# Kernel optimization log

Hardware: AMD Instinct MI355X
Metric: run time of the kernel (lower is better)

The kernel has to match this reference:

```python
import jax, jax.numpy as jnp
import numpy as np

CODEBOOK_SIZE = 8192
TOKEN_SIZE = 256
COMMITMENT_COST = 0.25
B, C, H, W = 32, 256, 32, 32


def setup_inputs() -> dict:
    key = jax.random.key(0)
    k1, k2 = jax.random.split(key)
    z = jax.random.normal(k1, (B, C, H, W), dtype=jnp.float32)
    # torch init: uniform_(-1/codebook_size, 1/codebook_size)
    embedding = jax.random.uniform(
        k2, (CODEBOOK_SIZE, TOKEN_SIZE), dtype=jnp.float32,
        minval=-1.0 / CODEBOOK_SIZE, maxval=1.0 / CODEBOOK_SIZE)
    return {"z": z, "embedding": embedding}


def reference(z, embedding):
    # b c h w -> b h w c
    z = jnp.transpose(z.astype(jnp.float32), (0, 2, 3, 1))
    b, h, w, c = z.shape
    z_flat = z.reshape(-1, c)  # [N, c]

    # squared euclidean distances: ||z||^2 + ||e||^2 - 2 z e^T
    d = (jnp.sum(z_flat ** 2, axis=1, keepdims=True)
         + jnp.sum(embedding ** 2, axis=1)
         - 2.0 * jnp.einsum('nd,kd->nk', z_flat, embedding))  # [N, K]
    idx = jnp.argmin(d, axis=1)  # [N]

    z_q = embedding[idx].reshape(z.shape)  # [b,h,w,c]

    commitment_loss = COMMITMENT_COST * jnp.mean(
        (jax.lax.stop_gradient(z_q) - z) ** 2)
    codebook_loss = jnp.mean((z_q - jax.lax.stop_gradient(z)) ** 2)
    loss = commitment_loss + codebook_loss

    # straight-through estimator
    z_q_st = z + jax.lax.stop_gradient(z_q - z)
    z_q_out = jnp.transpose(z_q_st, (0, 3, 1, 2))  # b h w c -> b c h w

    min_encoding_indices = idx.reshape(b, h, w)
    return (z_q_out, loss, commitment_loss, codebook_loss,
            min_encoding_indices)
```

## Files before the change

### kernel.cpp

```cpp
#include <hip/hip_runtime.h>
#include <float.h>

#define NBATCH 32
#define NCHAN  256
#define NHW    1024
#define NTOK   32768
#define NK     8192
#define ND     256
#define ZELEMS 8388608
#define OUT_LOSS 8388608
#define OUT_IDX  8388611
#define MARGIN   1.2e-4f

typedef short bf16x8  __attribute__((ext_vector_type(8)));
typedef float f32x4   __attribute__((ext_vector_type(4)));
typedef float f32x16  __attribute__((ext_vector_type(16)));

__device__ __forceinline__ void gl_lds16(const void* g, void* l) {
    __builtin_amdgcn_global_load_lds(
        (const __attribute__((address_space(1))) unsigned int*)g,
        (__attribute__((address_space(3))) unsigned int*)l, 16, 0, 0);
}

__device__ __forceinline__ unsigned short f2bf(float f) {
    unsigned int u = __float_as_uint(f);
    u += 0x7FFFu + ((u >> 16) & 1u);
    return (unsigned short)(u >> 16);
}

__device__ __forceinline__ float embed8(float x, int code) {
    return __int_as_float((__float_as_int(x) & 0xFFFFFF00) | code);
}


__global__ __launch_bounds__(256) void k_en(const float* __restrict__ E,
                                            float* __restrict__ en,
                                            float* __restrict__ acc,
                                            int* __restrict__ counter) {
    int t = threadIdx.x;
    int wv = t >> 6, lane = t & 63;
    int k = blockIdx.x * 4 + wv;
    const float4* E4 = (const float4*)E;
    float4 v = E4[k * 64 + lane];
    float s = v.x * v.x + v.y * v.y + v.z * v.z + v.w * v.w;
    #pragma unroll
    for (int off = 32; off > 0; off >>= 1) s += __shfl_down(s, off, 64);
    if (lane == 0) en[k] = s;
    if (blockIdx.x == 0 && t == 0) { acc[0] = 0.0f; counter[0] = 0; }
}

__global__ __launch_bounds__(256) void k_castE(const float* __restrict__ E,
                                               unsigned short* __restrict__ Epre) {
    int g = blockIdx.x * 256 + threadIdx.x;
    int code = g >> 5, c16 = g & 31;
    int kc = c16 >> 2, qlog = c16 & 3;
    int row = code & 127, tile = code >> 7;
    const float4* E4 = (const float4*)(E + code * ND + c16 * 8);
    float4 a = E4[0], b = E4[1];
    unsigned int u[4];
    u[0] = (unsigned int)f2bf(a.x) | ((unsigned int)f2bf(a.y) << 16);
    u[1] = (unsigned int)f2bf(a.z) | ((unsigned int)f2bf(a.w) << 16);
    u[2] = (unsigned int)f2bf(b.x) | ((unsigned int)f2bf(b.y) << 16);
    u[3] = (unsigned int)f2bf(b.z) | ((unsigned int)f2bf(b.w) << 16);
    int p = (qlog + (row >> 1)) & 3;
    *(uint4*)((char*)Epre + (size_t)(tile * 8 + kc) * 8192 + row * 64 + p * 16) =
        make_uint4(u[0], u[1], u[2], u[3]);
}

__global__ __launch_bounds__(256) void k_castZ(const float* __restrict__ zg,
                                               unsigned short* __restrict__ Zpre) {
    __shared__ unsigned short buf[128][34];
    int bi = blockIdx.x;
    int b = bi >> 6, kc = (bi >> 3) & 7, hwt = bi & 7;
    int c0 = kc * 32, hw0 = hwt * 128;
    int t = threadIdx.x;
    #pragma unroll
    for (int r = 0; r < 4; ++r) {
        int idx = r * 256 + t;
        int c = idx >> 5, q = idx & 31;
        float4 v = *(const float4*)&zg[(b * 256 + c0 + c) * 1024 + hw0 + q * 4];
        buf[q * 4 + 0][c] = f2bf(v.x);
        buf[q * 4 + 1][c] = f2bf(v.y);
        buf[q * 4 + 2][c] = f2bf(v.z);
        buf[q * 4 + 3][c] = f2bf(v.w);
    }
    __syncthreads();
    int row = t >> 1, half = t & 1;
    char* base = (char*)Zpre + (size_t)((b * 8 + hwt) * 8 + kc) * 8192 + row * 64;
    #pragma unroll
    for (int s = 0; s < 2; ++s) {
        int qlog = half * 2 + s;
        unsigned int u[4];
        #pragma unroll
        for (int k = 0; k < 4; ++k) {
            int cc = qlog * 8 + 2 * k;
            u[k] = (unsigned int)buf[row][cc] | ((unsigned int)buf[row][cc + 1] << 16);
        }
        int p = (qlog + (row >> 1)) & 3;
        *(uint4*)(base + p * 16) = make_uint4(u[0], u[1], u[2], u[3]);
    }
}

__global__ __launch_bounds__(256, 2) void k_dist(const unsigned short* __restrict__ Epre,
                                                 const unsigned short* __restrict__ Zpre,
                                                 const float* __restrict__ en,
                                                 float2* __restrict__ part2) {
    __shared__ __align__(16) char smem[2 * 24576];
    __shared__ float2 red[2][128];
    __shared__ float en_s[256];

    const int t    = threadIdx.x;
    const int kbb  = blockIdx.x;
    const int mb   = blockIdx.y;
    const int n0   = mb * 128;
    const int w    = t >> 6, lane = t & 63;
    const int l31  = lane & 31, lhi = lane >> 5;
    const int wm   = w >> 1, wn = w & 1;
    const int cA   = (lhi + (l31 >> 1)) & 3;

    en_s[t] = en[kbb * 256 + t];

    const char* Ebase = (const char*)Epre + (size_t)(kbb * 2) * 65536;
    const char* Zbase = (const char*)Zpre + (size_t)mb * 65536;

    auto stage = [&](int kc, int buf) {
        char* db = smem + buf * 24576;
        #pragma unroll
        for (int r = 0; r < 6; ++r) {
            int s = w * 6 + r;
            const char* src;
            if (s < 8)       src = Ebase + kc * 8192 + s * 1024;
            else if (s < 16) src = Ebase + 65536 + kc * 8192 + (s - 8) * 1024;
            else             src = Zbase + kc * 8192 + (s - 16) * 1024;
            gl_lds16(src + lane * 16, db + s * 1024 + lane * 16);
        }
    };

    f32x16 acc[2][2][2];
    #pragma unroll
    for (int kt = 0; kt < 2; ++kt)
        #pragma unroll
        for (int i = 0; i < 2; ++i)
            #pragma unroll
            for (int j = 0; j < 2; ++j) acc[kt][i][j] = (f32x16)0.0f;

    const int rowEoff = (wm * 64 + l31) * 64;
    const int rowZoff = 16384 + (wn * 64 + l31) * 64;
    const int colk[2] = { (cA & 3) * 16, (cA ^ 2) * 16 };

    stage(0, 0);
    for (int kc = 0; kc < 8; ++kc) {
        __syncthreads();
        if (kc < 7) stage(kc + 1, (kc + 1) & 1);
        char* db = smem + (kc & 1) * 24576;

        bf16x8 ea[2][2][2], zb[2][2];
        #pragma unroll
        for (int ks = 0; ks < 2; ++ks) {
            #pragma unroll
            for (int kt = 0; kt < 2; ++kt)
                #pragma unroll
                for (int i = 0; i < 2; ++i)
                    ea[kt][i][ks] = *(const bf16x8*)(db + kt * 8192 + rowEoff
                                                     + i * 2048 + colk[ks]);
            #pragma unroll
            for (int j = 0; j < 2; ++j)
                zb[j][ks] = *(const bf16x8*)(db + rowZoff + j * 2048 + colk[ks]);
        }
        #pragma unroll
        for (int kt = 0; kt < 2; ++kt)
            #pragma unroll
            for (int ks = 0; ks < 2; ++ks)
                #pragma unroll
                for (int i = 0; i < 2; ++i)
                    #pragma unroll
                    for (int j = 0; j < 2; ++j)
                        acc[kt][i][j] = __builtin_amdgcn_mfma_f32_32x32x16_bf16(
                            ea[kt][i][ks], zb[j][ks], acc[kt][i][j], 0, 0, 0);
    }

    float v1[2] = { FLT_MAX, FLT_MAX }, v2[2] = { FLT_MAX, FLT_MAX };
    #pragma unroll
    for (int kt = 0; kt < 2; ++kt)
        #pragma unroll
        for (int i = 0; i < 2; ++i) {
            const int cb = (kt << 7) | (wm << 6) | (i << 5) | (lhi << 2);
            #pragma unroll
            for (int rq = 0; rq < 4; ++rq) {
                f32x4 ev = *(const f32x4*)&en_s[cb + 8 * rq];
                #pragma unroll
                for (int rr = 0; rr < 4; ++rr) {
                    const int r = rq * 4 + rr;
                    const int code = cb + 8 * rq + rr;
                    #pragma unroll
                    for (int j = 0; j < 2; ++j) {
                        float s  = fmaf(-2.0f, acc[kt][i][j][r], ev[rr]);
                        float se = embed8(s, code);
                        v2[j] = __builtin_amdgcn_fmed3f(se, v1[j], v2[j]);
                        v1[j] = fminf(v1[j], se);
                    }
                }
            }
        }
    #pragma unroll
    for (int j = 0; j < 2; ++j) {
        float b1 = __shfl_xor(v1[j], 32, 64);
        float b2 = __shfl_xor(v2[j], 32, 64);
        float hi = fmaxf(v1[j], b1);
        v1[j] = fminf(v1[j], b1);
        v2[j] = fminf(fminf(hi, v2[j]), b2);
    }
    if (lane < 32) {
        #pragma unroll
        for (int j = 0; j < 2; ++j)
            red[wm][wn * 64 + j * 32 + lane] = make_float2(v1[j], v2[j]);
    }
    __syncthreads();
    if (t < 128) {
        float2 A = red[0][t], B = red[1][t];
        float g1 = fminf(A.x, B.x);
        float g2 = fminf(fminf(fmaxf(A.x, B.x), A.y), B.y);
        part2[(size_t)(n0 + t) * 32 + kbb] = make_float2(g1, g2);
    }
}

__global__ __launch_bounds__(256) void k_refine(const float* __restrict__ zg,
                                                const float* __restrict__ E,
                                                const float2* __restrict__ part2,
                                                int* __restrict__ idxw,
                                                float* __restrict__ outF) {
    const int w = threadIdx.x >> 6, l = threadIdx.x & 63;
    const int n = blockIdx.x * 4 + w;
    const int b = n >> 10, hw = n & 1023;
    const float* zrow = zg + b * (NCHAN * NHW) + hw;

    float zreg[4];
    #pragma unroll
    for (int j = 0; j < 4; ++j) zreg[j] = zrow[(4 * l + j) * NHW];

    double z2 = 0.0;
    #pragma unroll
    for (int j = 0; j < 4; ++j) z2 += (double)zreg[j] * (double)zreg[j];
    #pragma unroll
    for (int m = 1; m < 64; m <<= 1) z2 += __shfl_xor(z2, m, 64);
    const float z2f = (float)z2;

    float2 p = make_float2(FLT_MAX, FLT_MAX);
    if (l < 32) p = part2[(size_t)n * 32 + l];
    int code1 = (l << 8) | (__float_as_int(p.x) & 0xFF);
    int code2 = (l << 8) | (__float_as_int(p.y) & 0xFF);

    float vmin = p.x;
    #pragma unroll
    for (int m = 1; m < 64; m <<= 1) vmin = fminf(vmin, __shfl_xor(vmin, m, 64));
    const float thr = vmin + MARGIN;

    unsigned long long m1 = __ballot(l < 32 && p.x <= thr);
    unsigned long long m2 = __ballot(l < 32 && p.y <= thr);

    float bdq = FLT_MAX; int bidx = 0x7fffffff;
    #pragma unroll
    for (int pass = 0; pass < 2; ++pass) {
        unsigned long long mm = pass ? m2 : m1;
        int ibits = pass ? code2 : code1;
        while (mm) {
            int src = __ffsll(mm) - 1; mm &= mm - 1;
            int cidx = __shfl(ibits, src, 64);
            const float4 e4 = *(const float4*)&E[cidx * ND + 4 * l];
            double g = (double)zreg[0] * (double)e4.x + (double)zreg[1] * (double)e4.y
                     + (double)zreg[2] * (double)e4.z + (double)zreg[3] * (double)e4.w;
            #pragma unroll
            for (int mk = 1; mk < 64; mk <<= 1) g += __shfl_xor(g, mk, 64);
            float c  = (float)(2.0 * g);
            float dq = z2f - c;
            if (dq < bdq || (dq == bdq && cidx < bidx)) { bdq = dq; bidx = cidx; }
        }
    }
    if (l == 0) { idxw[n] = bidx; outF[OUT_IDX + n] = (float)bidx; }
}

__global__ __launch_bounds__(256) void k_gather(const float* __restrict__ E,
                                                const float* __restrict__ zg,
                                                const int* __restrict__ idxw,
                                                float* __restrict__ out,
                                                float* __restrict__ acc,
                                                int* __restrict__ counter) {
    __shared__ __align__(16) float Es[64 * 256];
    __shared__ int sidx[64];
    __shared__ float wred[4];
    const int t = threadIdx.x;
    const int b = blockIdx.x >> 4, ht = blockIdx.x & 15;

    if (t < 64) sidx[t] = idxw[b * 1024 + ht * 64 + t];
    __syncthreads();
    const float4* E4 = (const float4*)E;
    #pragma unroll
    for (int r = 0; r < 16; ++r) {
        int li = r * 256 + t;
        int row = li >> 6, slot = li & 63;
        float4 v = E4[(size_t)sidx[row] * 64 + slot];
        *(float4*)&Es[row * 256 + ((slot ^ (row & 15)) * 4)] = v;
    }
    __syncthreads();

    const int hw = t & 63, wv = t >> 6;
    float s = 0.0f;
    #pragma unroll 8
    for (int cc = 0; cc < 64; ++cc) {
        int c = wv * 64 + cc;
        float e = Es[hw * 256 + (((c >> 2) ^ (hw & 15)) * 4) + (c & 3)];
        size_t gi = (size_t)(b * 256 + c) * 1024 + ht * 64 + hw;
        float zv = zg[gi];
        out[gi] = e;
        float d = e - zv;
        s = fmaf(d, d, s);
    }
    #pragma unroll
    for (int off = 32; off > 0; off >>= 1) s += __shfl_down(s, off, 64);
    if ((t & 63) == 0) wred[wv] = s;
    __syncthreads();
    if (t == 0) {
        atomicAdd(acc, wred[0] + wred[1] + wred[2] + wred[3]);
        __threadfence();
        int old = atomicAdd(counter, 1);
        if (old == 511) {
            float total = atomicAdd(acc, 0.0f);
            float mse = total / 8388608.0f;
            out[OUT_LOSS + 0] = 1.25f * mse;
            out[OUT_LOSS + 1] = 0.25f * mse;
            out[OUT_LOSS + 2] = mse;
        }
    }
}

extern "C" void kernel_launch(void* const* d_in, const int* in_sizes, int n_in,
                              void* d_out, int out_size, void* d_ws, size_t ws_size,
                              hipStream_t stream) {
    const float* zg = (const float*)d_in[0];
    const float* E  = (const float*)d_in[1];
    float* out = (float*)d_out;
    float* wsf = (float*)d_ws;
    float*  acc     = wsf;
    int*    counter = (int*)(wsf + 1);
    float*  en      = wsf + 64;
    int*    idxw    = (int*)(wsf + 64 + NK);
    float2* part2   = (float2*)(wsf + 64 + NK + NTOK);
    unsigned short* Epre = (unsigned short*)(wsf + 64 + NK + NTOK + 2097152);
    unsigned short* Zpre = (unsigned short*)d_out;

    k_en    <<<NK / 4, 256, 0, stream>>>(E, en, acc, counter);
    k_castE <<<1024, 256, 0, stream>>>(E, Epre);
    k_castZ <<<2048, 256, 0, stream>>>(zg, Zpre);
    k_dist  <<<dim3(32, 256), 256, 0, stream>>>(Epre, Zpre, en, part2);
    k_refine<<<NTOK / 4, 256, 0, stream>>>(zg, E, part2, idxw, out);
    k_gather<<<512, 256, 0, stream>>>(E, zg, idxw, out, acc, counter);
}
```

Measured before the change: 348.0 us.

## Restructure VQ distance pipeline: register-resident codebook, smaller tiles, fused norms, batched refine

Folds the codebook-norm computation into the bf16 cast kernel, which removes one launch. Both packed layouts change to an MFMA-fragment-friendly order. The distance kernel now loads codebook fragments straight from global memory into registers with double buffering and stages only Z through LDS. It uses 128-code tiles, a doubled grid and 3 blocks per CU, which changes how much data each block reuses. The refine kernel transposes a 64-token z tile through shared memory so reads are coalesced instead of strided per token. The trade-off is more partial-minimum entries per token, twice as many codebook tiles read, and less reuse of Z per block.

After: 318.9 us. 1.09x faster.

```diff
diff --git a/kernel.cpp b/kernel.cpp
--- a/kernel.cpp
+++ b/kernel.cpp
@@ -33,38 +33,30 @@
 }
 
 
-__global__ __launch_bounds__(256) void k_en(const float* __restrict__ E,
-                                            float* __restrict__ en,
-                                            float* __restrict__ acc,
-                                            int* __restrict__ counter) {
-    int t = threadIdx.x;
-    int wv = t >> 6, lane = t & 63;
-    int k = blockIdx.x * 4 + wv;
-    const float4* E4 = (const float4*)E;
-    float4 v = E4[k * 64 + lane];
-    float s = v.x * v.x + v.y * v.y + v.z * v.z + v.w * v.w;
-    #pragma unroll
-    for (int off = 32; off > 0; off >>= 1) s += __shfl_down(s, off, 64);
-    if (lane == 0) en[k] = s;
-    if (blockIdx.x == 0 && t == 0) { acc[0] = 0.0f; counter[0] = 0; }
-}
-
 __global__ __launch_bounds__(256) void k_castE(const float* __restrict__ E,
-                                               unsigned short* __restrict__ Epre) {
+                                               unsigned short* __restrict__ Epre,
+                                               float* __restrict__ en,
+                                               float* __restrict__ acc,
+                                               int* __restrict__ counter) {
     int g = blockIdx.x * 256 + threadIdx.x;
     int code = g >> 5, c16 = g & 31;
-    int kc = c16 >> 2, qlog = c16 & 3;
-    int row = code & 127, tile = code >> 7;
+    int kc = c16 >> 2, ks = (c16 >> 1) & 1, lhi = c16 & 1;
     const float4* E4 = (const float4*)(E + code * ND + c16 * 8);
     float4 a = E4[0], b = E4[1];
+    float s = a.x*a.x + a.y*a.y + a.z*a.z + a.w*a.w
+            + b.x*b.x + b.y*b.y + b.z*b.z + b.w*b.w;
+    #pragma unroll
+    for (int off = 1; off < 32; off <<= 1) s += __shfl_xor(s, off, 64);
+    if ((threadIdx.x & 31) == 0) en[code] = s;
     unsigned int u[4];
     u[0] = (unsigned int)f2bf(a.x) | ((unsigned int)f2bf(a.y) << 16);
     u[1] = (unsigned int)f2bf(a.z) | ((unsigned int)f2bf(a.w) << 16);
     u[2] = (unsigned int)f2bf(b.x) | ((unsigned int)f2bf(b.y) << 16);
     u[3] = (unsigned int)f2bf(b.z) | ((unsigned int)f2bf(b.w) << 16);
-    int p = (qlog + (row >> 1)) & 3;
-    *(uint4*)((char*)Epre + (size_t)(tile * 8 + kc) * 8192 + row * 64 + p * 16) =
+    *(uint4*)((char*)Epre + (size_t)(code >> 7) * 65536 + kc * 8192
+              + (ks * 2 + lhi) * 2048 + (code & 127) * 16) =
         make_uint4(u[0], u[1], u[2], u[3]);
+    if (blockIdx.x == 0 && threadIdx.x == 0) { acc[0] = 0.0f; counter[0] = 0; }
 }
 
 __global__ __launch_bounds__(256) void k_castZ(const float* __restrict__ zg,
@@ -85,29 +77,28 @@
         buf[q * 4 + 3][c] = f2bf(v.w);
     }
     __syncthreads();
-    int row = t >> 1, half = t & 1;
-    char* base = (char*)Zpre + (size_t)((b * 8 + hwt) * 8 + kc) * 8192 + row * 64;
-    #pragma unroll
-    for (int s = 0; s < 2; ++s) {
-        int qlog = half * 2 + s;
+    int tok = t >> 1, ks = t & 1;
+    char* base = (char*)Zpre + (size_t)((b * 8 + hwt) * 8 + kc) * 8192;
+    #pragma unroll
+    for (int lhi = 0; lhi < 2; ++lhi) {
         unsigned int u[4];
         #pragma unroll
         for (int k = 0; k < 4; ++k) {
-            int cc = qlog * 8 + 2 * k;
-            u[k] = (unsigned int)buf[row][cc] | ((unsigned int)buf[row][cc + 1] << 16);
-        }
-        int p = (qlog + (row >> 1)) & 3;
-        *(uint4*)(base + p * 16) = make_uint4(u[0], u[1], u[2], u[3]);
-    }
-}
-
-__global__ __launch_bounds__(256, 2) void k_dist(const unsigned short* __restrict__ Epre,
+            int cc = ks * 16 + lhi * 8 + 2 * k;
+            u[k] = (unsigned int)buf[tok][cc] | ((unsigned int)buf[tok][cc + 1] << 16);
+        }
+        *(uint4*)(base + (ks * 2 + lhi) * 2048 + tok * 16) =
+            make_uint4(u[0], u[1], u[2], u[3]);
+    }
+}
+
+__global__ __launch_bounds__(256, 3) void k_dist(const unsigned short* __restrict__ Epre,
                                                  const unsigned short* __restrict__ Zpre,
                                                  const float* __restrict__ en,
                                                  float2* __restrict__ part2) {
-    __shared__ __align__(16) char smem[2 * 24576];
+    __shared__ __align__(16) char Zs[16384];
     __shared__ float2 red[2][128];
-    __shared__ float en_s[256];
+    __shared__ float en_s[128];
 
     const int t    = threadIdx.x;
     const int kbb  = blockIdx.x;
@@ -116,92 +107,86 @@
     const int w    = t >> 6, lane = t & 63;
     const int l31  = lane & 31, lhi = lane >> 5;
     const int wm   = w >> 1, wn = w & 1;
-    const int cA   = (lhi + (l31 >> 1)) & 3;
-
-    en_s[t] = en[kbb * 256 + t];
-
-    const char* Ebase = (const char*)Epre + (size_t)(kbb * 2) * 65536;
-    const char* Zbase = (const char*)Zpre + (size_t)mb * 65536;
+
+    if (t < 128) en_s[t] = en[kbb * 128 + t];
+
+    const char* Eb = (const char*)Epre + (size_t)kbb * 65536;
+    const char* Zb = (const char*)Zpre + (size_t)mb * 65536;
 
     auto stage = [&](int kc, int buf) {
-        char* db = smem + buf * 24576;
-        #pragma unroll
-        for (int r = 0; r < 6; ++r) {
-            int s = w * 6 + r;
-            const char* src;
-            if (s < 8)       src = Ebase + kc * 8192 + s * 1024;
-            else if (s < 16) src = Ebase + 65536 + kc * 8192 + (s - 8) * 1024;
-            else             src = Zbase + kc * 8192 + (s - 16) * 1024;
-            gl_lds16(src + lane * 16, db + s * 1024 + lane * 16);
+        char* db = Zs + buf * 8192;
+        #pragma unroll
+        for (int r = 0; r < 2; ++r) {
+            int s = w * 2 + r;
+            gl_lds16(Zb + kc * 8192 + s * 1024 + lane * 16,
+                     db + s * 1024 + lane * 16);
         }
     };
 
-    f32x16 acc[2][2][2];
-    #pragma unroll
-    for (int kt = 0; kt < 2; ++kt)
+    bf16x8 ea[2][2][2];
+    auto loadE = [&](int kc, int pp) {
         #pragma unroll
         for (int i = 0; i < 2; ++i)
             #pragma unroll
-            for (int j = 0; j < 2; ++j) acc[kt][i][j] = (f32x16)0.0f;
-
-    const int rowEoff = (wm * 64 + l31) * 64;
-    const int rowZoff = 16384 + (wn * 64 + l31) * 64;
-    const int colk[2] = { (cA & 3) * 16, (cA ^ 2) * 16 };
-
+            for (int ks = 0; ks < 2; ++ks)
+                ea[pp][i][ks] = *(const bf16x8*)(Eb + kc * 8192
+                    + (ks * 2 + lhi) * 2048 + (wm * 64 + i * 32 + l31) * 16);
+    };
+
+    f32x16 acc[2][2];
+    #pragma unroll
+    for (int i = 0; i < 2; ++i)
+        #pragma unroll
+        for (int j = 0; j < 2; ++j) acc[i][j] = (f32x16)0.0f;
+
+    loadE(0, 0);
     stage(0, 0);
+    #pragma unroll
     for (int kc = 0; kc < 8; ++kc) {
         __syncthreads();
-        if (kc < 7) stage(kc + 1, (kc + 1) & 1);
-        char* db = smem + (kc & 1) * 24576;
-
-        bf16x8 ea[2][2][2], zb[2][2];
-        #pragma unroll
-        for (int ks = 0; ks < 2; ++ks) {
-            #pragma unroll
-            for (int kt = 0; kt < 2; ++kt)
-                #pragma unroll
-                for (int i = 0; i < 2; ++i)
-                    ea[kt][i][ks] = *(const bf16x8*)(db + kt * 8192 + rowEoff
-                                                     + i * 2048 + colk[ks]);
-            #pragma unroll
-            for (int j = 0; j < 2; ++j)
-                zb[j][ks] = *(const bf16x8*)(db + rowZoff + j * 2048 + colk[ks]);
-        }
-        #pragma unroll
-        for (int kt = 0; kt < 2; ++kt)
+        if (kc < 7) {
+            stage(kc + 1, (kc + 1) & 1);
+            loadE(kc + 1, (kc + 1) & 1);
+        }
+        const char* zbuf = Zs + (kc & 1) * 8192;
+        bf16x8 zb[2][2];
+        #pragma unroll
+        for (int j = 0; j < 2; ++j)
             #pragma unroll
             for (int ks = 0; ks < 2; ++ks)
+                zb[j][ks] = *(const bf16x8*)(zbuf + (ks * 2 + lhi) * 2048
+                                             + (wn * 64 + j * 32 + l31) * 16);
+        #pragma unroll
+        for (int ks = 0; ks < 2; ++ks)
+            #pragma unroll
+            for (int i = 0; i < 2; ++i)
                 #pragma unroll
-                for (int i = 0; i < 2; ++i)
-                    #pragma unroll
-                    for (int j = 0; j < 2; ++j)
-                        acc[kt][i][j] = __builtin_amdgcn_mfma_f32_32x32x16_bf16(
-                            ea[kt][i][ks], zb[j][ks], acc[kt][i][j], 0, 0, 0);
+                for (int j = 0; j < 2; ++j)
+                    acc[i][j] = __builtin_amdgcn_mfma_f32_32x32x16_bf16(
+                        ea[kc & 1][i][ks], zb[j][ks], acc[i][j], 0, 0, 0);
     }
 
     float v1[2] = { FLT_MAX, FLT_MAX }, v2[2] = { FLT_MAX, FLT_MAX };
     #pragma unroll
-    for (int kt = 0; kt < 2; ++kt)
-        #pragma unroll
-        for (int i = 0; i < 2; ++i) {
-            const int cb = (kt << 7) | (wm << 6) | (i << 5) | (lhi << 2);
+    for (int i = 0; i < 2; ++i) {
+        const int cb = (wm << 6) | (i << 5) | (lhi << 2);
+        #pragma unroll
+        for (int rq = 0; rq < 4; ++rq) {
+            f32x4 ev = *(const f32x4*)&en_s[cb + 8 * rq];
             #pragma unroll
-            for (int rq = 0; rq < 4; ++rq) {
-                f32x4 ev = *(const f32x4*)&en_s[cb + 8 * rq];
+            for (int rr = 0; rr < 4; ++rr) {
+                const int r = rq * 4 + rr;
+                const int code = cb + 8 * rq + rr;
                 #pragma unroll
-                for (int rr = 0; rr < 4; ++rr) {
-                    const int r = rq * 4 + rr;
-                    const int code = cb + 8 * rq + rr;
-                    #pragma unroll
-                    for (int j = 0; j < 2; ++j) {
-                        float s  = fmaf(-2.0f, acc[kt][i][j][r], ev[rr]);
-                        float se = embed8(s, code);
-                        v2[j] = __builtin_amdgcn_fmed3f(se, v1[j], v2[j]);
-                        v1[j] = fminf(v1[j], se);
-                    }
+                for (int j = 0; j < 2; ++j) {
+                    float s  = fmaf(-2.0f, acc[i][j][r], ev[rr]);
+                    float se = embed8(s, code);
+                    v2[j] = __builtin_amdgcn_fmed3f(se, v1[j], v2[j]);
+                    v1[j] = fminf(v1[j], se);
                 }
             }
         }
+    }
     #pragma unroll
     for (int j = 0; j < 2; ++j) {
         float b1 = __shfl_xor(v1[j], 32, 64);
@@ -220,7 +205,7 @@
         float2 A = red[0][t], B = red[1][t];
         float g1 = fminf(A.x, B.x);
         float g2 = fminf(fminf(fmaxf(A.x, B.x), A.y), B.y);
-        part2[(size_t)(n0 + t) * 32 + kbb] = make_float2(g1, g2);
+        part2[(size_t)(n0 + t) * 64 + kbb] = make_float2(g1, g2);
     }
 }
 
@@ -229,54 +214,73 @@
                                                 const float2* __restrict__ part2,
                                                 int* __restrict__ idxw,
                                                 float* __restrict__ outF) {
-    const int w = threadIdx.x >> 6, l = threadIdx.x & 63;
-    const int n = blockIdx.x * 4 + w;
-    const int b = n >> 10, hw = n & 1023;
-    const float* zrow = zg + b * (NCHAN * NHW) + hw;
-
-    float zreg[4];
-    #pragma unroll
-    for (int j = 0; j < 4; ++j) zreg[j] = zrow[(4 * l + j) * NHW];
-
-    double z2 = 0.0;
-    #pragma unroll
-    for (int j = 0; j < 4; ++j) z2 += (double)zreg[j] * (double)zreg[j];
-    #pragma unroll
-    for (int m = 1; m < 64; m <<= 1) z2 += __shfl_xor(z2, m, 64);
-    const float z2f = (float)z2;
-
-    float2 p = make_float2(FLT_MAX, FLT_MAX);
-    if (l < 32) p = part2[(size_t)n * 32 + l];
-    int code1 = (l << 8) | (__float_as_int(p.x) & 0xFF);
-    int code2 = (l << 8) | (__float_as_int(p.y) & 0xFF);
-
-    float vmin = p.x;
-    #pragma unroll
-    for (int m = 1; m < 64; m <<= 1) vmin = fminf(vmin, __shfl_xor(vmin, m, 64));
-    const float thr = vmin + MARGIN;
-
-    unsigned long long m1 = __ballot(l < 32 && p.x <= thr);
-    unsigned long long m2 = __ballot(l < 32 && p.y <= thr);
-
-    float bdq = FLT_MAX; int bidx = 0x7fffffff;
-    #pragma unroll
-    for (int pass = 0; pass < 2; ++pass) {
-        unsigned long long mm = pass ? m2 : m1;
-        int ibits = pass ? code2 : code1;
-        while (mm) {
-            int src = __ffsll(mm) - 1; mm &= mm - 1;
-            int cidx = __shfl(ibits, src, 64);
-            const float4 e4 = *(const float4*)&E[cidx * ND + 4 * l];
-            double g = (double)zreg[0] * (double)e4.x + (double)zreg[1] * (double)e4.y
-                     + (double)zreg[2] * (double)e4.z + (double)zreg[3] * (double)e4.w;
-            #pragma unroll
-            for (int mk = 1; mk < 64; mk <<= 1) g += __shfl_xor(g, mk, 64);
-            float c  = (float)(2.0 * g);
-            float dq = z2f - c;
-            if (dq < bdq || (dq == bdq && cidx < bidx)) { bdq = dq; bidx = cidx; }
-        }
-    }
-    if (l == 0) { idxw[n] = bidx; outF[OUT_IDX + n] = (float)bidx; }
+    __shared__ float Zs[256 * 65];
+    const int t = threadIdx.x;
+    const int n0 = blockIdx.x * 64;
+    const int b = n0 >> 10, hw0 = n0 & 1023;
+
+    #pragma unroll
+    for (int r = 0; r < 16; ++r) {
+        int li = r * 256 + t;
+        int c = li >> 4, q = li & 15;
+        float4 v = *(const float4*)&zg[(b * 256 + c) * 1024 + hw0 + q * 4];
+        Zs[c * 65 + q * 4 + 0] = v.x;
+        Zs[c * 65 + q * 4 + 1] = v.y;
+        Zs[c * 65 + q * 4 + 2] = v.z;
+        Zs[c * 65 + q * 4 + 3] = v.w;
+    }
+    __syncthreads();
+
+    const int w = t >> 6, l = t & 63;
+    for (int it = 0; it < 16; ++it) {
+        const int tokl = w * 16 + it;
+        const int n = n0 + tokl;
+
+        float zreg[4];
+        #pragma unroll
+        for (int j = 0; j < 4; ++j) zreg[j] = Zs[(64 * j + l) * 65 + tokl];
+
+        double z2 = 0.0;
+        #pragma unroll
+        for (int j = 0; j < 4; ++j) z2 += (double)zreg[j] * (double)zreg[j];
+        #pragma unroll
+        for (int m = 1; m < 64; m <<= 1) z2 += __shfl_xor(z2, m, 64);
+        const float z2f = (float)z2;
+
+        float2 p = part2[(size_t)n * 64 + l];
+        int code1 = (l << 7) | (__float_as_int(p.x) & 0x7F);
+        int code2 = (l << 7) | (__float_as_int(p.y) & 0x7F);
+
+        float vmin = p.x;
+        #pragma unroll
+        for (int m = 1; m < 64; m <<= 1) vmin = fminf(vmin, __shfl_xor(vmin, m, 64));
+        const float thr = vmin + MARGIN;
+
+        unsigned long long m1 = __ballot(p.x <= thr);
+        unsigned long long m2 = __ballot(p.y <= thr);
+
+        float bdq = FLT_MAX; int bidx = 0x7fffffff;
+        #pragma unroll
+        for (int pass = 0; pass < 2; ++pass) {
+            unsigned long long mm = pass ? m2 : m1;
+            int ibits = pass ? code2 : code1;
+            while (mm) {
+                int src = __ffsll(mm) - 1; mm &= mm - 1;
+                int cidx = __shfl(ibits, src, 64);
+                const float* erow = E + cidx * ND;
+                double g = (double)zreg[0] * (double)erow[l]
+                         + (double)zreg[1] * (double)erow[64 + l]
+                         + (double)zreg[2] * (double)erow[128 + l]
+                         + (double)zreg[3] * (double)erow[192 + l];
+                #pragma unroll
+                for (int mk = 1; mk < 64; mk <<= 1) g += __shfl_xor(g, mk, 64);
+                float c  = (float)(2.0 * g);
+                float dq = z2f - c;
+                if (dq < bdq || (dq == bdq && cidx < bidx)) { bdq = dq; bidx = cidx; }
+            }
+        }
+        if (l == 0) { idxw[n] = bidx; outF[OUT_IDX + n] = (float)bidx; }
+    }
 }
 
 __global__ __launch_bounds__(256) void k_gather(const float* __restrict__ E,
@@ -345,13 +349,12 @@
     float*  en      = wsf + 64;
     int*    idxw    = (int*)(wsf + 64 + NK);
     float2* part2   = (float2*)(wsf + 64 + NK + NTOK);
-    unsigned short* Epre = (unsigned short*)(wsf + 64 + NK + NTOK + 2097152);
+    unsigned short* Epre = (unsigned short*)(wsf + 64 + NK + NTOK + 4194304);
     unsigned short* Zpre = (unsigned short*)d_out;
 
-    k_en    <<<NK / 4, 256, 0, stream>>>(E, en, acc, counter);
-    k_castE <<<1024, 256, 0, stream>>>(E, Epre);
+    k_castE <<<1024, 256, 0, stream>>>(E, Epre, en, acc, counter);
     k_castZ <<<2048, 256, 0, stream>>>(zg, Zpre);
-    k_dist  <<<dim3(32, 256), 256, 0, stream>>>(Epre, Zpre, en, part2);
-    k_refine<<<NTOK / 4, 256, 0, stream>>>(zg, E, part2, idxw, out);
+    k_dist  <<<dim3(64, 256), 256, 0, stream>>>(Epre, Zpre, en, part2);
+    k_refine<<<NTOK / 64, 256, 0, stream>>>(zg, E, part2, idxw, out);
     k_gather<<<512, 256, 0, stream>>>(E, zg, idxw, out, acc, counter);
 }
```
